# Kernel tuning notes

Hardware: AMD Instinct MI355X
Metric: run time of the kernel (lower is better)

Reference implementation:

```python
import jax, jax.numpy as jnp
import numpy as np

N_NODES = 32768
N_EDGES = 65536
NODE_IN = 4
EDGE_IN = 4
HIDDEN = 64
LN_EPS = 1e-5


def setup_inputs() -> dict:
    key = jax.random.key(0)
    ks = jax.random.split(key, 20)
    s = 0.05
    inp = {
        "x": jax.random.normal(ks[0], (N_NODES, NODE_IN), dtype=jnp.float32),
        "edge_attr": jax.random.normal(ks[1], (N_EDGES, EDGE_IN), dtype=jnp.float32),
        "edge_index": jax.random.randint(ks[2], (2, N_EDGES), 0, N_NODES, dtype=jnp.int64),
        "batch": jnp.zeros((N_NODES,), dtype=jnp.int64),
        # layer 1: edge MLP edge_in->64->node_in*hidden, root [node_in,hidden]
        "e1_w1": jax.random.normal(ks[3], (EDGE_IN, 64), dtype=jnp.float32) * s,
        "e1_b1": jnp.zeros((64,), jnp.float32),
        "e1_w2": jax.random.normal(ks[4], (64, NODE_IN * HIDDEN), dtype=jnp.float32) * s,
        "e1_b2": jnp.zeros((NODE_IN * HIDDEN,), jnp.float32),
        "root1": jax.random.normal(ks[5], (NODE_IN, HIDDEN), dtype=jnp.float32) * s,
        "bias1": jnp.zeros((HIDDEN,), jnp.float32),
        "ln1_g": jnp.ones((HIDDEN,), jnp.float32),
        "ln1_b": jnp.zeros((HIDDEN,), jnp.float32),
        # layer 2: edge MLP edge_in->128->hidden*hidden, root [hidden,hidden]
        "e2_w1": jax.random.normal(ks[6], (EDGE_IN, 128), dtype=jnp.float32) * s,
        "e2_b1": jnp.zeros((128,), jnp.float32),
        "e2_w2": jax.random.normal(ks[7], (128, HIDDEN * HIDDEN), dtype=jnp.float32) * s,
        "e2_b2": jnp.zeros((HIDDEN * HIDDEN,), jnp.float32),
        "root2": jax.random.normal(ks[8], (HIDDEN, HIDDEN), dtype=jnp.float32) * s,
        "bias2": jnp.zeros((HIDDEN,), jnp.float32),
        "ln2_g": jnp.ones((HIDDEN,), jnp.float32),
        "ln2_b": jnp.zeros((HIDDEN,), jnp.float32),
    }
    return inp


def _nnconv(x, src, dst, edge_attr, ew1, eb1, ew2, eb2, root, bias, n_nodes):
    # edge-conditioned weights: [E, in_ch, out_ch]
    in_ch = x.shape[1]
    out_ch = root.shape[1]
    h = jax.nn.relu(edge_attr @ ew1 + eb1) @ ew2 + eb2
    W = h.reshape(-1, in_ch, out_ch)
    # gather source features, per-edge matvec, scatter-mean to dest
    msg = jnp.einsum('ei,eio->eo', x[src], W)  # [E, out_ch]
    summed = jax.ops.segment_sum(msg, dst, num_segments=n_nodes)
    cnt = jax.ops.segment_sum(jnp.ones((dst.shape[0],), msg.dtype), dst,
                              num_segments=n_nodes)
    agg = summed / jnp.maximum(cnt, 1.0)[:, None]
    return agg + x @ root + bias


def _layernorm(x, g, b):
    m = x.mean(-1, keepdims=True)
    v = ((x - m) ** 2).mean(-1, keepdims=True)
    return (x - m) * jax.lax.rsqrt(v + LN_EPS) * g + b


def reference(x, edge_attr, e1_w1, e1_b1, e1_w2, e1_b2, root1, bias1, ln1_g, ln1_b,
              e2_w1, e2_b1, e2_w2, e2_b2, root2, bias2, ln2_g, ln2_b,
              edge_index, batch):
    src, dst = edge_index[0], edge_index[1]
    n = x.shape[0]
    h = _nnconv(x, src, dst, edge_attr, e1_w1, e1_b1, e1_w2, e1_b2, root1, bias1, n)
    h = _layernorm(jax.nn.relu(h), ln1_g, ln1_b)  # dropout = identity (eval)
    h = _nnconv(h, src, dst, edge_attr, e2_w1, e2_b1, e2_w2, e2_b2, root2, bias2, n)
    h = _layernorm(jax.nn.relu(h), ln2_g, ln2_b)
    # global mean pool (single graph -> [1, hidden])
    gs = jax.ops.segment_sum(h, batch, num_segments=1)
    gc = jax.ops.segment_sum(jnp.ones((n,), h.dtype), batch, num_segments=1)
    return gs / jnp.maximum(gc, 1.0)[:, None]
```

## Files before the change

kernel.cpp:

```cpp
#include <hip/hip_runtime.h>

#define N_NODES 32768
#define N_EDGES 65536

typedef float f32x4 __attribute__((ext_vector_type(4)));
typedef float f32x2 __attribute__((ext_vector_type(2)));
typedef short s16x8 __attribute__((ext_vector_type(8)));

__device__ __forceinline__ unsigned short f2bf(float f){
  unsigned u = __float_as_uint(f);
  u += 0x7FFFu + ((u >> 16) & 1u);
  return (unsigned short)(u >> 16);
}
__device__ __forceinline__ float bf2f(unsigned short b){
  return __uint_as_float(((unsigned)b) << 16);
}

__global__ void k_prep(const float* __restrict__ e2_w2, const float* __restrict__ e2_b2,
                       const float* __restrict__ e1_w2,
                       unsigned short* __restrict__ W2f, unsigned short* __restrict__ T1g,
                       int* __restrict__ cz){
  __shared__ float S[4096];
  const int b = blockIdx.x, tid = threadIdx.x;
  if (b < 129){
    const float* src = (b < 128) ? (e2_w2 + b * 4096) : e2_b2;
    #pragma unroll
    for (int t = 0; t < 4096; t += 256) S[t + tid] = src[t + tid];
    __syncthreads();
    #pragma unroll
    for (int t = 0; t < 4096; t += 256){
      int u = t + tid;
      int j = u & 7, l = (u >> 3) & 63, half = (u >> 9) & 1, ot = (u >> 10) & 3;
      int i = half * 32 + ((l >> 4) << 3) + j;
      int o = ot * 16 + (l & 15);
      W2f[b * 4096 + u] = f2bf(S[i * 64 + o]);
    }
  } else if (b < 193){
    int t = (b - 129) * 256 + tid;
    int j = t & 7, l = (t >> 3) & 63, half = (t >> 9) & 1, ot = (t >> 10) & 3, i = t >> 12;
    int kf = half * 32 + ((l >> 4) << 3) + j;
    int o = ot * 16 + (l & 15);
    T1g[t] = f2bf(e1_w2[kf * 256 + i * 64 + o]);
  } else {
    int z = (b - 193) * 256 + tid;
    if (z < 65536) cz[z] = 0;
  }
}

__global__ void k_hist(const int* __restrict__ ei, int* __restrict__ cnti){
  int i = blockIdx.x * 256 + threadIdx.x;
  if (i < N_EDGES) atomicAdd(cnti + ei[N_EDGES + i], 1);
}

__global__ void k_scanA(const int* __restrict__ cnti, int* __restrict__ lex, int* __restrict__ bsum){
  const int tid = threadIdx.x;
  int n = blockIdx.x * 256 + tid;
  int c = cnti[n];
  int v = c;
  int lane = tid & 63;
  #pragma unroll
  for (int d = 1; d < 64; d <<= 1){
    int t = __shfl_up(v, d);
    if (lane >= d) v += t;
  }
  __shared__ int wsum[4];
  if (lane == 63) wsum[tid >> 6] = v;
  __syncthreads();
  int off = 0;
  for (int i = 0; i < (tid >> 6); ++i) off += wsum[i];
  lex[n] = off + v - c;
  if (tid == 255) bsum[blockIdx.x] = off + v;
}

__global__ void k_fill(const int* __restrict__ ei, const int* __restrict__ lex,
                       const int* __restrict__ bsum, int* __restrict__ cur,
                       int* __restrict__ eslot, int* __restrict__ bsx){
  __shared__ int sb[128];
  __shared__ int w0s;
  const int tid = threadIdx.x;
  const int lane = tid & 63;
  int c = 0, v = 0;
  if (tid < 128){
    c = bsum[tid];
    v = c;
    #pragma unroll
    for (int d = 1; d < 64; d <<= 1){
      int t = __shfl_up(v, d);
      if (lane >= d) v += t;
    }
  }
  if (tid == 63) w0s = v;
  __syncthreads();
  if (tid < 128) sb[tid] = v + ((tid >= 64) ? w0s : 0) - c;
  __syncthreads();
  if (blockIdx.x == 0 && tid < 128) bsx[tid] = sb[tid];
  int e = blockIdx.x * 256 + tid;
  int d = ei[N_EDGES + e];
  int base = lex[d] + sb[d >> 8];
  eslot[e] = base + atomicAdd(cur + d, 1);
}

__launch_bounds__(256, 4)
__global__ void k_msg1(const float* __restrict__ x, const float* __restrict__ ea,
                       const int* __restrict__ ei, const int* __restrict__ eslot,
                       const float* __restrict__ e1_w1, const float* __restrict__ e1_b1,
                       const float* __restrict__ e1_b2,
                       const unsigned short* __restrict__ T1g,
                       unsigned short* __restrict__ msg1b)
{
  __shared__ float eas[64 * 4];
  __shared__ unsigned short F1f[8 * 64 * 8];
  const int tid = threadIdx.x;
  const int eblk = blockIdx.x * 64;

  if (tid < 64) ((float4*)eas)[tid] = ((const float4*)ea)[eblk + tid];
  __syncthreads();
  {
    int kf = tid & 63, eh = tid >> 6;
    float w0 = e1_w1[kf], w1 = e1_w1[64 + kf], w2 = e1_w1[128 + kf], w3 = e1_w1[192 + kf];
    float bb = e1_b1[kf];
    int half = kf >> 5, hi = (kf >> 3) & 3, j = kf & 7;
    for (int e = eh * 16; e < eh * 16 + 16; ++e){
      float s = fmaf(eas[e*4+0], w0, fmaf(eas[e*4+1], w1, fmaf(eas[e*4+2], w2, fmaf(eas[e*4+3], w3, bb))));
      F1f[(((e >> 4) * 2 + half) * 64 + hi * 16 + (e & 15)) * 8 + j] = f2bf(fmaxf(s, 0.f));
    }
  }
  __syncthreads();

  const int l = tid & 63, lm = l & 15, lg = l >> 4;
  const int ot = tid >> 6;
  int esl[4];
  float xs[4][4];
  s16x8 bf[4][2];
  #pragma unroll
  for (int et = 0; et < 4; ++et){
    int e = eblk + et * 16 + lm;
    int s = ei[e];
    esl[et] = eslot[e];
    float4 xv = *(const float4*)(x + s * 4);
    xs[et][0] = xv.x; xs[et][1] = xv.y; xs[et][2] = xv.z; xs[et][3] = xv.w;
    bf[et][0] = ((const s16x8*)F1f)[(et * 2 + 0) * 64 + l];
    bf[et][1] = ((const s16x8*)F1f)[(et * 2 + 1) * 64 + l];
  }
  f32x4 acc[4];
  #pragma unroll
  for (int et = 0; et < 4; ++et) acc[et] = (f32x4){0.f, 0.f, 0.f, 0.f};

  #pragma unroll
  for (int i = 0; i < 4; ++i){
    const s16x8* p = (const s16x8*)(T1g + (i * 4 + ot) * 1024);
    s16x8 a0 = p[l], a1 = p[64 + l];
    #pragma unroll
    for (int et = 0; et < 4; ++et){
      f32x4 g = (f32x4){0.f, 0.f, 0.f, 0.f};
      g = __builtin_amdgcn_mfma_f32_16x16x32_bf16(a0, bf[et][0], g, 0, 0, 0);
      g = __builtin_amdgcn_mfma_f32_16x16x32_bf16(a1, bf[et][1], g, 0, 0, 0);
      acc[et] += xs[et][i] * g;
    }
  }
  float b2v[4][4];
  #pragma unroll
  for (int i = 0; i < 4; ++i)
    #pragma unroll
    for (int r = 0; r < 4; ++r) b2v[i][r] = e1_b2[i * 64 + ot * 16 + lg * 4 + r];
  #pragma unroll
  for (int et = 0; et < 4; ++et)
    #pragma unroll
    for (int r = 0; r < 4; ++r)
      #pragma unroll
      for (int i = 0; i < 4; ++i) acc[et][r] = fmaf(xs[et][i], b2v[i][r], acc[et][r]);

  #pragma unroll
  for (int et = 0; et < 4; ++et){
    unsigned p0 = ((unsigned)f2bf(acc[et][1]) << 16) | f2bf(acc[et][0]);
    unsigned p1 = ((unsigned)f2bf(acc[et][3]) << 16) | f2bf(acc[et][2]);
    *(uint2*)(msg1b + (size_t)esl[et] * 64 + ot * 16 + lg * 4) = make_uint2(p0, p1);
  }
}

__launch_bounds__(256)
__global__ void k_node1(const float* __restrict__ x, const float* __restrict__ root1,
                        const float* __restrict__ bias1, const float* __restrict__ lng,
                        const float* __restrict__ lnb, const int* __restrict__ cnti,
                        const int* __restrict__ lex, const int* __restrict__ bsx,
                        const unsigned short* __restrict__ msg1b, unsigned short* __restrict__ h1b)
{
  const int tid = threadIdx.x;
  int n = blockIdx.x * 4 + (tid >> 6);
  int o = tid & 63;
  int rp = lex[n] + bsx[n >> 8];
  int deg = cnti[n];
  float s = 0.f;
  for (int j = 0; j < deg; ++j) s += bf2f(msg1b[(size_t)(rp + j) * 64 + o]);
  float v = s * (1.f / fmaxf((float)deg, 1.f));
  float4 xv = *(const float4*)(x + n * 4);
  v = fmaf(xv.x, root1[o], v);
  v = fmaf(xv.y, root1[64 + o], v);
  v = fmaf(xv.z, root1[128 + o], v);
  v = fmaf(xv.w, root1[192 + o], v);
  v = fmaxf(v + bias1[o], 0.f);
  float m = v;
  #pragma unroll
  for (int d = 32; d > 0; d >>= 1) m += __shfl_xor(m, d);
  m *= (1.f / 64.f);
  float dd = v - m;
  float var = dd * dd;
  #pragma unroll
  for (int d = 32; d > 0; d >>= 1) var += __shfl_xor(var, d);
  var *= (1.f / 64.f);
  float out = dd * rsqrtf(var + 1e-5f) * lng[o] + lnb[o];
  h1b[n * 64 + o] = f2bf(out);
}

__launch_bounds__(512, 4)
__global__ void k_msg2(const float* __restrict__ ea, const int* __restrict__ ei,
                       const int* __restrict__ eslot,
                       const float* __restrict__ e2_w1, const float* __restrict__ e2_b1,
                       const unsigned short* __restrict__ h1b,
                       const unsigned short* __restrict__ W2f,
                       float* __restrict__ msg)
{
  __shared__ float eas[128 * 4];
  __shared__ float F2s[128 * 132];
  const int tid = threadIdx.x;
  const int eblk = blockIdx.x * 128;
  const int w = tid >> 6, l = tid & 63, lm = l & 15, lg = l >> 4;
  const int ot = w >> 1, eh = w & 1;

  int esl[4];
  s16x8 bh[4][2];
  #pragma unroll
  for (int et = 0; et < 4; ++et){
    int eloc = eh * 64 + et * 16 + lm;
    int e = eblk + eloc;
    int s = ei[e];
    esl[et] = eslot[e];
    const s16x8* hp = (const s16x8*)(h1b + s * 64);
    bh[et][0] = hp[lg];
    bh[et][1] = hp[4 + lg];
  }

  if (tid < 128) ((float4*)eas)[tid] = ((const float4*)ea)[eblk + tid];
  __syncthreads();
  {
    int kf = tid & 127, q = tid >> 7;
    float w0 = e2_w1[kf], w1 = e2_w1[128 + kf], w2 = e2_w1[256 + kf], w3 = e2_w1[384 + kf];
    float bb = e2_b1[kf];
    for (int e = q * 32; e < q * 32 + 32; ++e){
      float s = fmaf(eas[e*4+0], w0, fmaf(eas[e*4+1], w1, fmaf(eas[e*4+2], w2, fmaf(eas[e*4+3], w3, bb))));
      F2s[e * 132 + kf] = fmaxf(s, 0.f);
    }
  }
  __syncthreads();

  f32x2 accL[4], accH[4];
  #pragma unroll
  for (int et = 0; et < 4; ++et){ accL[et] = (f32x2){0.f, 0.f}; accH[et] = (f32x2){0.f, 0.f}; }

  const int voff = ot * 2048 + l * 16;
  s16x8 A0[2], A1[2], A2[2], A3[2];

#define LOADA(DST, KF) { \
    const unsigned short* sb = W2f + (size_t)(KF) * 4096; \
    asm volatile("global_load_dwordx4 %0, %2, %3\n\t" \
                 "global_load_dwordx4 %1, %2, %3 offset:1024" \
      : "=&v"(DST[0]), "=&v"(DST[1]) : "v"(voff), "s"(sb)); }
#define WAITA(N) do { asm volatile("s_waitcnt vmcnt(" #N ")"); \
                      __builtin_amdgcn_sched_barrier(0); } while(0);
#define STEP(A, J) { \
    __builtin_amdgcn_s_setprio(1); \
    _Pragma("unroll") \
    for (int et = 0; et < 4; ++et){ \
      f32x4 g = (f32x4){0.f, 0.f, 0.f, 0.f}; \
      g = __builtin_amdgcn_mfma_f32_16x16x32_bf16(A[0], bh[et][0], g, 0, 0, 0); \
      g = __builtin_amdgcn_mfma_f32_16x16x32_bf16(A[1], bh[et][1], g, 0, 0, 0); \
      float fs = f2c[et][J]; \
      f32x2 ff = (f32x2){fs, fs}; \
      f32x2 glo = __builtin_shufflevector(g, g, 0, 1); \
      f32x2 ghi = __builtin_shufflevector(g, g, 2, 3); \
      accL[et] = __builtin_elementwise_fma(glo, ff, accL[et]); \
      accH[et] = __builtin_elementwise_fma(ghi, ff, accH[et]); \
    } \
    __builtin_amdgcn_s_setprio(0); }

  LOADA(A0, 0)
  LOADA(A1, 1)
  LOADA(A2, 2)
  LOADA(A3, 3)
  #pragma unroll 1
  for (int kf = 0; kf < 128; kf += 4){
    f32x4 f2c[4];
    #pragma unroll
    for (int et = 0; et < 4; ++et)
      f2c[et] = *(const f32x4*)&F2s[(eh * 64 + et * 16 + lm) * 132 + kf];
    const int k5 = (kf + 5 > 128) ? 128 : kf + 5;
    const int k6 = (kf + 6 > 128) ? 128 : kf + 6;
    const int k7 = (kf + 7 > 128) ? 128 : kf + 7;
    WAITA(6) STEP(A0, 0) LOADA(A0, kf + 4)
    WAITA(6) STEP(A1, 1) LOADA(A1, k5)
    WAITA(6) STEP(A2, 2) LOADA(A2, k6)
    WAITA(6) STEP(A3, 3) LOADA(A3, k7)
  }
  WAITA(0)
  #pragma unroll
  for (int et = 0; et < 4; ++et){
    f32x4 g = (f32x4){0.f, 0.f, 0.f, 0.f};
    g = __builtin_amdgcn_mfma_f32_16x16x32_bf16(A0[0], bh[et][0], g, 0, 0, 0);
    g = __builtin_amdgcn_mfma_f32_16x16x32_bf16(A0[1], bh[et][1], g, 0, 0, 0);
    accL[et] += __builtin_shufflevector(g, g, 0, 1);
    accH[et] += __builtin_shufflevector(g, g, 2, 3);
  }
#undef LOADA
#undef WAITA
#undef STEP

  #pragma unroll
  for (int et = 0; et < 4; ++et){
    f32x4 o4;
    o4[0] = accL[et][0]; o4[1] = accL[et][1];
    o4[2] = accH[et][0]; o4[3] = accH[et][1];
    *(f32x4*)(msg + (size_t)esl[et] * 64 + ot * 16 + lg * 4) = o4;
  }
}

__launch_bounds__(1024)
__global__ void k_node2(const unsigned short* __restrict__ h1b, const float* __restrict__ root2,
                        const float* __restrict__ bias2, const float* __restrict__ lng,
                        const float* __restrict__ lnb, const int* __restrict__ cnti,
                        const int* __restrict__ lex, const int* __restrict__ bsx,
                        const float* __restrict__ msg, float* __restrict__ partial)
{
  const int tid = threadIdx.x;
  const int q = tid >> 6, o = tid & 63;
  float tsum = 0.f;
  #pragma unroll 1
  for (int it = 0; it < 4; ++it){
    int n = blockIdx.x * 64 + it * 16 + q;
    int rp = lex[n] + bsx[n >> 8];
    int deg = cnti[n];
    float s = 0.f;
    for (int j = 0; j < deg; ++j) s += msg[(size_t)(rp + j) * 64 + o];
    float v = s * (1.f / fmaxf((float)deg, 1.f));
    const s16x8* hp = (const s16x8*)(h1b + n * 64);
    #pragma unroll
    for (int c = 0; c < 8; ++c){
      s16x8 hv = hp[c];
      #pragma unroll
      for (int j = 0; j < 8; ++j)
        v = fmaf(bf2f((unsigned short)hv[j]), root2[(c * 8 + j) * 64 + o], v);
    }
    v = fmaxf(v + bias2[o], 0.f);
    float m = v;
    #pragma unroll
    for (int d = 32; d > 0; d >>= 1) m += __shfl_xor(m, d);
    m *= (1.f / 64.f);
    float dd = v - m;
    float var = dd * dd;
    #pragma unroll
    for (int d = 32; d > 0; d >>= 1) var += __shfl_xor(var, d);
    var *= (1.f / 64.f);
    tsum += dd * rsqrtf(var + 1e-5f) * lng[o] + lnb[o];
  }
  __shared__ float pp[16][64];
  pp[q][o] = tsum;
  __syncthreads();
  if (tid < 64){
    float t = 0.f;
    #pragma unroll
    for (int k = 0; k < 16; ++k) t += pp[k][tid];
    partial[blockIdx.x * 64 + tid] = t;
  }
}

__launch_bounds__(1024)
__global__ void k_out(const float* __restrict__ partial, float* __restrict__ out){
  const int tid = threadIdx.x;
  int o = tid & 63, q = tid >> 6;
  float s = 0.f;
  for (int b = q; b < 512; b += 16) s += partial[b * 64 + o];
  __shared__ float pp[16][64];
  pp[q][o] = s;
  __syncthreads();
  if (tid < 64){
    float t = 0.f;
    #pragma unroll
    for (int k = 0; k < 16; ++k) t += pp[k][tid];
    out[tid] = t * (1.f / 32768.f);
  }
}

extern "C" void kernel_launch(void* const* d_in, const int* in_sizes, int n_in,
                              void* d_out, int out_size, void* d_ws, size_t ws_size,
                              hipStream_t stream)
{
  const float* x      = (const float*)d_in[0];
  const float* ea     = (const float*)d_in[1];
  const int*   ei     = (const int*)  d_in[2];
  const float* e1_w1  = (const float*)d_in[4];
  const float* e1_b1  = (const float*)d_in[5];
  const float* e1_w2  = (const float*)d_in[6];
  const float* e1_b2  = (const float*)d_in[7];
  const float* root1  = (const float*)d_in[8];
  const float* bias1  = (const float*)d_in[9];
  const float* ln1g   = (const float*)d_in[10];
  const float* ln1b   = (const float*)d_in[11];
  const float* e2_w1  = (const float*)d_in[12];
  const float* e2_b1  = (const float*)d_in[13];
  const float* e2_w2  = (const float*)d_in[14];
  const float* e2_b2  = (const float*)d_in[15];
  const float* root2  = (const float*)d_in[16];
  const float* bias2  = (const float*)d_in[17];
  const float* ln2g   = (const float*)d_in[18];
  const float* ln2b   = (const float*)d_in[19];

  char* w = (char*)d_ws;
  float*          msg     = (float*)(w);
  unsigned short* msg1b   = (unsigned short*)(w);
  unsigned short* h1b     = (unsigned short*)(w + 16777216);
  unsigned short* W2f     = (unsigned short*)(w + 20971520);
  unsigned short* T1g     = (unsigned short*)(w + 22028288);
  int*            cnti    = (int*)(w + 22061056);
  int*            cur     = (int*)(w + 22192128);
  int*            lex     = (int*)(w + 22323200);
  int*            bsx     = (int*)(w + 22454272);
  int*            bsum    = (int*)(w + 22454784);
  int*            eslot   = (int*)(w + 22455296);
  float*          partial = (float*)(w + 22717440);

  k_prep <<<449, 256, 0, stream>>>(e2_w2, e2_b2, e1_w2, W2f, T1g, cnti);
  k_hist <<<256, 256, 0, stream>>>(ei, cnti);
  k_scanA<<<128, 256, 0, stream>>>(cnti, lex, bsum);
  k_fill <<<256, 256, 0, stream>>>(ei, lex, bsum, cur, eslot, bsx);
  k_msg1 <<<1024, 256, 0, stream>>>(x, ea, ei, eslot, e1_w1, e1_b1, e1_b2, T1g, msg1b);
  k_node1<<<8192, 256, 0, stream>>>(x, root1, bias1, ln1g, ln1b, cnti, lex, bsx, msg1b, h1b);
  k_msg2 <<<512, 512, 0, stream>>>(ea, ei, eslot, e2_w1, e2_b1, h1b, W2f, msg);
  k_node2<<<512, 1024, 0, stream>>>(h1b, root2, bias2, ln2g, ln2b, cnti, lex, bsx, msg, partial);
  k_out  <<<1, 1024, 0, stream>>>(partial, (float*)d_out);
}
```

Baseline: 153.2 us.

## Split k_msg2 input-channel reduction across two waves with LDS combine

```diff
diff --git a/kernel.cpp b/kernel.cpp
--- a/kernel.cpp
+++ b/kernel.cpp
@@ -212,7 +212,7 @@
   h1b[n * 64 + o] = f2bf(out);
 }
 
-__launch_bounds__(512, 4)
+__launch_bounds__(1024)
 __global__ void k_msg2(const float* __restrict__ ea, const int* __restrict__ ei,
                        const int* __restrict__ eslot,
                        const float* __restrict__ e2_w1, const float* __restrict__ e2_b1,
@@ -225,19 +225,17 @@
   const int tid = threadIdx.x;
   const int eblk = blockIdx.x * 128;
   const int w = tid >> 6, l = tid & 63, lm = l & 15, lg = l >> 4;
-  const int ot = w >> 1, eh = w & 1;
+  const int ot = w >> 2, eh = (w >> 1) & 1, ki = w & 1;
 
   int esl[4];
-  s16x8 bh[4][2];
+  s16x8 bh[4];
   #pragma unroll
   for (int et = 0; et < 4; ++et){
     int eloc = eh * 64 + et * 16 + lm;
     int e = eblk + eloc;
     int s = ei[e];
     esl[et] = eslot[e];
-    const s16x8* hp = (const s16x8*)(h1b + s * 64);
-    bh[et][0] = hp[lg];
-    bh[et][1] = hp[4 + lg];
+    bh[et] = ((const s16x8*)(h1b + s * 64))[ki * 4 + lg];
   }
 
   if (tid < 128) ((float4*)eas)[tid] = ((const float4*)ea)[eblk + tid];
@@ -246,7 +244,7 @@
     int kf = tid & 127, q = tid >> 7;
     float w0 = e2_w1[kf], w1 = e2_w1[128 + kf], w2 = e2_w1[256 + kf], w3 = e2_w1[384 + kf];
     float bb = e2_b1[kf];
-    for (int e = q * 32; e < q * 32 + 32; ++e){
+    for (int e = q * 16; e < q * 16 + 16; ++e){
       float s = fmaf(eas[e*4+0], w0, fmaf(eas[e*4+1], w1, fmaf(eas[e*4+2], w2, fmaf(eas[e*4+3], w3, bb))));
       F2s[e * 132 + kf] = fmaxf(s, 0.f);
     }
@@ -257,14 +255,13 @@
   #pragma unroll
   for (int et = 0; et < 4; ++et){ accL[et] = (f32x2){0.f, 0.f}; accH[et] = (f32x2){0.f, 0.f}; }
 
-  const int voff = ot * 2048 + l * 16;
-  s16x8 A0[2], A1[2], A2[2], A3[2];
+  const int voff = ot * 2048 + ki * 1024 + l * 16;
+  s16x8 A0, A1, A2, A3;
 
 #define LOADA(DST, KF) { \
     const unsigned short* sb = W2f + (size_t)(KF) * 4096; \
-    asm volatile("global_load_dwordx4 %0, %2, %3\n\t" \
-                 "global_load_dwordx4 %1, %2, %3 offset:1024" \
-      : "=&v"(DST[0]), "=&v"(DST[1]) : "v"(voff), "s"(sb)); }
+    asm volatile("global_load_dwordx4 %0, %1, %2" \
+      : "=&v"(DST) : "v"(voff), "s"(sb)); }
 #define WAITA(N) do { asm volatile("s_waitcnt vmcnt(" #N ")"); \
                       __builtin_amdgcn_sched_barrier(0); } while(0);
 #define STEP(A, J) { \
@@ -272,8 +269,7 @@
     _Pragma("unroll") \
     for (int et = 0; et < 4; ++et){ \
       f32x4 g = (f32x4){0.f, 0.f, 0.f, 0.f}; \
-      g = __builtin_amdgcn_mfma_f32_16x16x32_bf16(A[0], bh[et][0], g, 0, 0, 0); \
-      g = __builtin_amdgcn_mfma_f32_16x16x32_bf16(A[1], bh[et][1], g, 0, 0, 0); \
+      g = __builtin_amdgcn_mfma_f32_16x16x32_bf16(A, bh[et], g, 0, 0, 0); \
       float fs = f2c[et][J]; \
       f32x2 ff = (f32x2){fs, fs}; \
       f32x2 glo = __builtin_shufflevector(g, g, 0, 1); \
@@ -296,17 +292,16 @@
     const int k5 = (kf + 5 > 128) ? 128 : kf + 5;
     const int k6 = (kf + 6 > 128) ? 128 : kf + 6;
     const int k7 = (kf + 7 > 128) ? 128 : kf + 7;
-    WAITA(6) STEP(A0, 0) LOADA(A0, kf + 4)
-    WAITA(6) STEP(A1, 1) LOADA(A1, k5)
-    WAITA(6) STEP(A2, 2) LOADA(A2, k6)
-    WAITA(6) STEP(A3, 3) LOADA(A3, k7)
+    WAITA(3) STEP(A0, 0) LOADA(A0, kf + 4)
+    WAITA(3) STEP(A1, 1) LOADA(A1, k5)
+    WAITA(3) STEP(A2, 2) LOADA(A2, k6)
+    WAITA(3) STEP(A3, 3) LOADA(A3, k7)
   }
   WAITA(0)
   #pragma unroll
   for (int et = 0; et < 4; ++et){
     f32x4 g = (f32x4){0.f, 0.f, 0.f, 0.f};
-    g = __builtin_amdgcn_mfma_f32_16x16x32_bf16(A0[0], bh[et][0], g, 0, 0, 0);
-    g = __builtin_amdgcn_mfma_f32_16x16x32_bf16(A0[1], bh[et][1], g, 0, 0, 0);
+    g = __builtin_amdgcn_mfma_f32_16x16x32_bf16(A0, bh[et], g, 0, 0, 0);
     accL[et] += __builtin_shufflevector(g, g, 0, 1);
     accH[et] += __builtin_shufflevector(g, g, 2, 3);
   }
@@ -314,12 +309,27 @@
 #undef WAITA
 #undef STEP
 
-  #pragma unroll
-  for (int et = 0; et < 4; ++et){
-    f32x4 o4;
-    o4[0] = accL[et][0]; o4[1] = accL[et][1];
-    o4[2] = accH[et][0]; o4[3] = accH[et][1];
-    *(f32x4*)(msg + (size_t)esl[et] * 64 + ot * 16 + lg * 4) = o4;
+  __syncthreads();
+  float* red = (float*)F2s;
+  if (ki == 1){
+    #pragma unroll
+    for (int et = 0; et < 4; ++et){
+      f32x4 o4;
+      o4[0] = accL[et][0]; o4[1] = accL[et][1];
+      o4[2] = accH[et][0]; o4[3] = accH[et][1];
+      *(f32x4*)&red[(((ot * 2 + eh) * 4 + et) * 64 + l) * 4] = o4;
+    }
+  }
+  __syncthreads();
+  if (ki == 0){
+    #pragma unroll
+    for (int et = 0; et < 4; ++et){
+      f32x4 p = *(const f32x4*)&red[(((ot * 2 + eh) * 4 + et) * 64 + l) * 4];
+      f32x4 o4;
+      o4[0] = accL[et][0] + p[0]; o4[1] = accL[et][1] + p[1];
+      o4[2] = accH[et][0] + p[2]; o4[3] = accH[et][1] + p[3];
+      *(f32x4*)(msg + (size_t)esl[et] * 64 + ot * 16 + lg * 4) = o4;
+    }
   }
 }
 
@@ -433,7 +443,7 @@
   k_fill <<<256, 256, 0, stream>>>(ei, lex, bsum, cur, eslot, bsx);
   k_msg1 <<<1024, 256, 0, stream>>>(x, ea, ei, eslot, e1_w1, e1_b1, e1_b2, T1g, msg1b);
   k_node1<<<8192, 256, 0, stream>>>(x, root1, bias1, ln1g, ln1b, cnti, lex, bsx, msg1b, h1b);
-  k_msg2 <<<512, 512, 0, stream>>>(ea, ei, eslot, e2_w1, e2_b1, h1b, W2f, msg);
+  k_msg2 <<<512, 1024, 0, stream>>>(ea, ei, eslot, e2_w1, e2_b1, h1b, W2f, msg);
   k_node2<<<512, 1024, 0, stream>>>(h1b, root2, bias2, ln2g, ln2b, cnti, lex, bsx, msg, partial);
   k_out  <<<1, 1024, 0, stream>>>(partial, (float*)d_out);
 }
```

Measured after the change: 168.9 us. 10.2% more time.

## Fuse prep, histogram, scan and slot-fill kernels into one cooperative kernel

Applied to the files above, without the earlier changes.

```diff
diff --git a/kernel.cpp b/kernel.cpp
--- a/kernel.cpp
+++ b/kernel.cpp
@@ -1,4 +1,7 @@
 #include <hip/hip_runtime.h>
+#include <hip/hip_cooperative_groups.h>
+
+namespace cg = cooperative_groups;
 
 #define N_NODES 32768
 #define N_EDGES 65536
@@ -16,17 +19,25 @@
   return __uint_as_float(((unsigned)b) << 16);
 }
 
-__global__ void k_prep(const float* __restrict__ e2_w2, const float* __restrict__ e2_b2,
-                       const float* __restrict__ e1_w2,
-                       unsigned short* __restrict__ W2f, unsigned short* __restrict__ T1g,
-                       int* __restrict__ cz){
+__global__ void k_setup(const float* __restrict__ e2_w2, const float* __restrict__ e2_b2,
+                        const float* __restrict__ e1_w2,
+                        unsigned short* __restrict__ W2f, unsigned short* __restrict__ T1g,
+                        const int* __restrict__ ei, int* __restrict__ cz ,
+                        int* __restrict__ cur,
+                        int* __restrict__ lex, int* __restrict__ bsx,
+                        int* __restrict__ bsum, int* __restrict__ eslot)
+{
+  cg::grid_group grid = cg::this_grid();
   __shared__ float S[4096];
+  __shared__ int sb[136];
   const int b = blockIdx.x, tid = threadIdx.x;
+
   if (b < 129){
     const float* src = (b < 128) ? (e2_w2 + b * 4096) : e2_b2;
     #pragma unroll
     for (int t = 0; t < 4096; t += 256) S[t + tid] = src[t + tid];
     __syncthreads();
+    grid.sync();
     #pragma unroll
     for (int t = 0; t < 4096; t += 256){
       int u = t + tid;
@@ -35,69 +46,60 @@
       int o = ot * 16 + (l & 15);
       W2f[b * 4096 + u] = f2bf(S[i * 64 + o]);
     }
+    grid.sync();
+    grid.sync();
   } else if (b < 193){
     int t = (b - 129) * 256 + tid;
     int j = t & 7, l = (t >> 3) & 63, half = (t >> 9) & 1, ot = (t >> 10) & 3, i = t >> 12;
     int kf = half * 32 + ((l >> 4) << 3) + j;
     int o = ot * 16 + (l & 15);
     T1g[t] = f2bf(e1_w2[kf * 256 + i * 64 + o]);
+    grid.sync();
+    grid.sync();
+    grid.sync();
   } else {
-    int z = (b - 193) * 256 + tid;
-    if (z < 65536) cz[z] = 0;
-  }
-}
-
-__global__ void k_hist(const int* __restrict__ ei, int* __restrict__ cnti){
-  int i = blockIdx.x * 256 + threadIdx.x;
-  if (i < N_EDGES) atomicAdd(cnti + ei[N_EDGES + i], 1);
-}
-
-__global__ void k_scanA(const int* __restrict__ cnti, int* __restrict__ lex, int* __restrict__ bsum){
-  const int tid = threadIdx.x;
-  int n = blockIdx.x * 256 + tid;
-  int c = cnti[n];
-  int v = c;
-  int lane = tid & 63;
-  #pragma unroll
-  for (int d = 1; d < 64; d <<= 1){
-    int t = __shfl_up(v, d);
-    if (lane >= d) v += t;
-  }
-  __shared__ int wsum[4];
-  if (lane == 63) wsum[tid >> 6] = v;
-  __syncthreads();
-  int off = 0;
-  for (int i = 0; i < (tid >> 6); ++i) off += wsum[i];
-  lex[n] = off + v - c;
-  if (tid == 255) bsum[blockIdx.x] = off + v;
-}
-
-__global__ void k_fill(const int* __restrict__ ei, const int* __restrict__ lex,
-                       const int* __restrict__ bsum, int* __restrict__ cur,
-                       int* __restrict__ eslot, int* __restrict__ bsx){
-  __shared__ int sb[128];
-  __shared__ int w0s;
-  const int tid = threadIdx.x;
-  const int lane = tid & 63;
-  int c = 0, v = 0;
-  if (tid < 128){
-    c = bsum[tid];
-    v = c;
-    #pragma unroll
-    for (int d = 1; d < 64; d <<= 1){
-      int t = __shfl_up(v, d);
-      if (lane >= d) v += t;
-    }
-  }
-  if (tid == 63) w0s = v;
-  __syncthreads();
-  if (tid < 128) sb[tid] = v + ((tid >= 64) ? w0s : 0) - c;
-  __syncthreads();
-  if (blockIdx.x == 0 && tid < 128) bsx[tid] = sb[tid];
-  int e = blockIdx.x * 256 + tid;
-  int d = ei[N_EDGES + e];
-  int base = lex[d] + sb[d >> 8];
-  eslot[e] = base + atomicAdd(cur + d, 1);
+    const int idx = (b - 193) * 256 + tid;
+    cz[idx] = 0;
+    grid.sync();
+    const int d = ei[N_EDGES + idx];
+    atomicAdd(cz + d, 1);
+    grid.sync();
+    if (b < 321){
+      int n = idx;
+      int c = cz[n];
+      int v = c;
+      int lane = tid & 63;
+      #pragma unroll
+      for (int dd = 1; dd < 64; dd <<= 1){
+        int t2 = __shfl_up(v, dd);
+        if (lane >= dd) v += t2;
+      }
+      if (lane == 63) sb[128 + (tid >> 6)] = v;
+      __syncthreads();
+      int off = 0;
+      for (int i = 0; i < (tid >> 6); ++i) off += sb[128 + i];
+      lex[n] = off + v - c;
+      if (tid == 255) bsum[b - 193] = off + v;
+    }
+    grid.sync();
+    if (tid < 128) sb[tid] = bsum[tid];
+    __syncthreads();
+    int c128 = (tid < 128) ? sb[tid] : 0;
+    int v = c128;
+    int lane = tid & 63;
+    #pragma unroll
+    for (int dd = 1; dd < 64; dd <<= 1){
+      int t2 = __shfl_up(v, dd);
+      if (lane >= dd) v += t2;
+    }
+    if (tid == 63) sb[132] = v;
+    __syncthreads();
+    if (tid < 128) sb[tid] = v + ((tid >= 64) ? sb[132] : 0) - c128;
+    __syncthreads();
+    if (b == 193 && tid < 128) bsx[tid] = sb[tid];
+    int base = lex[d] + sb[d >> 8];
+    eslot[idx] = base + atomicAdd(cur + d, 1);
+  }
 }
 
 __launch_bounds__(256, 4)
@@ -427,10 +429,15 @@
   int*            eslot   = (int*)(w + 22455296);
   float*          partial = (float*)(w + 22717440);
 
-  k_prep <<<449, 256, 0, stream>>>(e2_w2, e2_b2, e1_w2, W2f, T1g, cnti);
-  k_hist <<<256, 256, 0, stream>>>(ei, cnti);
-  k_scanA<<<128, 256, 0, stream>>>(cnti, lex, bsum);
-  k_fill <<<256, 256, 0, stream>>>(ei, lex, bsum, cur, eslot, bsx);
+  {
+    const float* a0 = e2_w2; const float* a1 = e2_b2; const float* a2 = e1_w2;
+    unsigned short* a3 = W2f; unsigned short* a4 = T1g;
+    const int* a5 = ei; int* a6 = cnti; int* a7 = cur;
+    int* a8 = lex; int* a9 = bsx; int* a10 = bsum; int* a11 = eslot;
+    void* args[] = {&a0, &a1, &a2, &a3, &a4, &a5, &a6, &a7, &a8, &a9, &a10, &a11};
+    hipLaunchCooperativeKernel(reinterpret_cast<void*>(k_setup), dim3(449), dim3(256),
+                               args, 0, stream);
+  }
   k_msg1 <<<1024, 256, 0, stream>>>(x, ea, ei, eslot, e1_w1, e1_b1, e1_b2, T1g, msg1b);
   k_node1<<<8192, 256, 0, stream>>>(x, root1, bias1, ln1g, ln1b, cnti, lex, bsx, msg1b, h1b);
   k_msg2 <<<512, 512, 0, stream>>>(ea, ei, eslot, e2_w1, e2_b1, h1b, W2f, msg);
```

New measurement: 304.5 us. +98.8%, slower.
